# Kernel optimization log

Measured on AMD Instinct MI355X. Metric: run time of the kernel, lower is better.

Reference implementation:

```python
import jax, jax.numpy as jnp
import numpy as np

NUM_CLASSES = 22
H_IMG, W_IMG = 256, 320
VOTE_STEPS = 160          # number of discrete steps each pixel votes along its ray
VOTE_THRESH = 0.5         # inlier threshold used by HoughVoterPyTorch


def setup_inputs() -> dict:
    key = jax.random.key(0)
    ks = jax.random.split(key, 24)
    B = 4
    rn = lambda k, s, sc=1.0: (jax.random.normal(k, s, jnp.float32) * sc)
    inp = {
        'x1': rn(ks[0], (B, 512, 8, 10)),
        'x2': rn(ks[1], (B, 256, 16, 20)),
        'x3': rn(ks[2], (B, 128, 32, 40)),
        'x4': rn(ks[3], (B, 64, 64, 80)),
        'x5': rn(ks[4], (B, 64, 128, 160)),
        'depth': jax.random.uniform(ks[5], (B, 1, H_IMG, W_IMG), jnp.float32, 0.5, 3.0),
    }
    raw = jax.random.uniform(ks[6], (B, NUM_CLASSES, H_IMG, W_IMG), jnp.float32)
    inp['seg'] = jnp.where(raw > 0.97, raw, 0.0)  # sparse per-class responses
    inp['fx'] = jnp.float32(572.4); inp['fy'] = jnp.float32(573.6)
    inp['px'] = jnp.float32(W_IMG / 2); inp['py'] = jnp.float32(H_IMG / 2)
    # ConvTranspose2d weights in torch layout [Cin, Cout, kH, kW]
    inp['w5'] = rn(ks[7], (512, 256, 4, 4), 0.02); inp['b5'] = jnp.zeros((256,), jnp.float32)
    inp['w4'] = rn(ks[8], (512, 128, 4, 4), 0.02); inp['b4'] = jnp.zeros((128,), jnp.float32)
    inp['w3'] = rn(ks[9], (256, 64, 4, 4), 0.03);  inp['b3'] = jnp.zeros((64,), jnp.float32)
    inp['w2'] = rn(ks[10], (128, 64, 4, 4), 0.04); inp['b2'] = jnp.zeros((64,), jnp.float32)
    inp['w1'] = rn(ks[11], (128, 64, 4, 4), 0.04); inp['b1'] = jnp.zeros((64,), jnp.float32)
    inp['wv'] = rn(ks[12], (3 * NUM_CLASSES, 64), 0.1); inp['bv'] = jnp.zeros((3 * NUM_CLASSES,), jnp.float32)
    inp['wc'] = rn(ks[13], (NUM_CLASSES, 64), 0.1);     inp['bc'] = jnp.zeros((NUM_CLASSES,), jnp.float32)
    return inp


def conv_t(x, w, b):
    # torch ConvTranspose2d(k=4, s=2, p=1) == dilated conv with flipped kernel
    k = jnp.flip(w, (2, 3)).transpose(1, 0, 2, 3)  # [Cout, Cin, 4, 4]
    y = jax.lax.conv_general_dilated(x, k, (1, 1), ((2, 2), (2, 2)),
                                     lhs_dilation=(2, 2),
                                     dimension_numbers=('NCHW', 'OIHW', 'NCHW'))
    return y + b[None, :, None, None]


def hough_vote(seg2d, dirs, depth2d, fx, fy, px, py):
    # seg2d: [H,W] fused fg prob; dirs: [H,W,2] (dx,dy); depth2d: [H,W]
    H, W = seg2d.shape
    n = dirs / (jnp.linalg.norm(dirs, axis=-1, keepdims=True) + 1e-6)
    u = n[..., 0].reshape(-1)
    v = n[..., 1].reshape(-1)
    ys, xs = jnp.meshgrid(jnp.arange(H, dtype=jnp.float32),
                          jnp.arange(W, dtype=jnp.float32), indexing='ij')
    xs = xs.reshape(-1); ys = ys.reshape(-1)
    w = (seg2d * (seg2d > VOTE_THRESH)).reshape(-1)  # weighted fg votes

    def step(acc, t):
        xt = jnp.round(xs + t * u).astype(jnp.int32)
        yt = jnp.round(ys + t * v).astype(jnp.int32)
        inb = (xt >= 0) & (xt < W) & (yt >= 0) & (yt < H)
        idx = jnp.clip(yt, 0, H - 1) * W + jnp.clip(xt, 0, W - 1)
        return acc.at[idx].add(jnp.where(inb, w, 0.0)), None

    acc, _ = jax.lax.scan(step, jnp.zeros(H * W, jnp.float32),
                          jnp.arange(1, VOTE_STEPS + 1, dtype=jnp.float32))
    vote_map = acc.reshape(H, W)
    ci = jnp.argmax(acc)
    cy = (ci // W).astype(jnp.float32)
    cx = (ci % W).astype(jnp.float32)
    mask = (seg2d > VOTE_THRESH).astype(jnp.float32)
    tz = jnp.sum(depth2d * mask) / (jnp.sum(mask) + 1e-6)
    tx = (cx - px) * tz / fx
    ty = (cy - py) * tz / fy
    return vote_map, jnp.stack([cx, cy]), jnp.stack([tx, ty, tz])


def reference(x1, x2, x3, x4, x5, depth, seg, fx, fy, px, py,
              w5, b5, w4, b4, w3, b3, w2, b2, w1, b1, wv, bv, wc, bc):
    x = jax.nn.relu(conv_t(x1, w5, b5))
    x = jax.nn.relu(conv_t(jnp.concatenate([x, x2], 1), w4, b4))
    x = jax.nn.relu(conv_t(jnp.concatenate([x, x3], 1), w3, b3))
    x = jax.nn.relu(conv_t(jnp.concatenate([x, x4], 1), w2, b2))
    x = jax.nn.relu(conv_t(jnp.concatenate([x, x5], 1), w1, b1))
    bottom_vertex = jnp.einsum('bchw,oc->bohw', x, wv) + bv[None, :, None, None]
    logits = jnp.einsum('bchw,oc->bohw', x, wc) + bc[None, :, None, None]
    bottom_label = jnp.argmax(logits, axis=1)
    center_dirs = jnp.transpose(bottom_vertex[:, :2], (0, 2, 3, 1))  # [B,H,W,2]
    seg_fused = jnp.clip(jnp.sum(seg, axis=1), 0.0, 1.0)             # [B,H,W]
    vote_maps, centers, translations = jax.vmap(
        hough_vote, in_axes=(0, 0, 0, None, None, None, None)
    )(seg_fused, center_dirs, depth[:, 0], fx, fy, px, py)
    return bottom_vertex, bottom_label, vote_maps, centers, translations
```

## Files before the change

kernel.cpp:

```cpp
#include <hip/hip_runtime.h>
#include <cstdint>
#include <cstddef>

#define H_IMG 256
#define W_IMG 320
#define HW_IMG (H_IMG * W_IMG)
#define NCLS 22
#define VOTE_STEPS 160

__global__ void repack_kernel(const float* __restrict__ w, double* __restrict__ wp,
                              int CIN, int COUT) {
    int total = CIN * COUT * 16;
    for (int i = blockIdx.x * blockDim.x + threadIdx.x; i < total;
         i += gridDim.x * blockDim.x) {
        int j = i & 3;
        int co = (i >> 2) % COUT;
        int rest = (i >> 2) / COUT;
        int cin = rest % CIN;
        int pp = rest / CIN;
        int ry = pp >> 1, rx = pp & 1;
        int dy = j >> 1, dx = j & 1;
        int ky = 3 - ry - 2 * dy;
        int kx = 3 - rx - 2 * dx;
        wp[i] = (double)w[((size_t)cin * COUT + co) * 16 + ky * 4 + kx];
    }
}

__global__ void repackR_kernel(const float* __restrict__ w, double* __restrict__ wr,
                               int CIN, int COUT) {
    int NCOG = COUT >> 4;
    int total = CIN * COUT * 16;
    for (int i = blockIdx.x * blockDim.x + threadIdx.x; i < total;
         i += gridDim.x * blockDim.x) {
        int tap = i & 3;
        int co = (i >> 2) & 15;
        int rest = i >> 6;
        int cin = rest % CIN;
        int pc = rest / CIN;
        int cog = pc % NCOG;
        int pp = pc / NCOG;
        int ry = pp >> 1, rx = pp & 1;
        int dy = tap >> 1, dxx = tap & 1;
        int ky = 3 - ry - 2 * dy;
        int kx = 3 - rx - 2 * dxx;
        wr[i] = (double)w[((size_t)cin * COUT + (cog * 16 + co)) * 16 + ky * 4 + kx];
    }
}

__global__ void transpose_d_kernel(const float* __restrict__ w, double* __restrict__ wt,
                                   int O, int K) {
    int i = blockIdx.x * blockDim.x + threadIdx.x;
    if (i < O * K) {
        int o = i / K, k = i - o * K;
        wt[k * O + o] = (double)w[i];
    }
}

template <bool RELU_A, bool ADBL>
__global__ __launch_bounds__(256) void convt_part_kernel(
    const void* __restrict__ inA_, int CA,
    const float* __restrict__ inB, int CB,
    const double* __restrict__ wp,
    double* __restrict__ parts,
    int COUT, int Hin, int Win, int nSplit, int B, int TOT) {
    const int NCO = 16;
    const int CIN = CA + CB;
    const int cog = blockIdx.y >> 2;
    const int pp = blockIdx.y & 3;
    const int ry = pp >> 1, rx = pp & 1;
    const int b = blockIdx.z % B;
    const int sp = blockIdx.z / B;
    const int cinPer = CIN / nSplit;
    const int c0 = sp * cinPer, c1 = c0 + cinPer;
    const int co0 = cog * NCO;
    const int plane = Hin * Win;
    const int Hout = Hin * 2, Wout = Win * 2;
    double* out = parts + (size_t)sp * TOT;

    __shared__ double wl[64 * 64];
    for (int i = threadIdx.x; i < cinPer * 64; i += 256) {
        int ci = i >> 6, k = i & 63;
        wl[i] = wp[(((size_t)pp * CIN + c0 + ci) * COUT + co0) * 4 + k];
    }
    __syncthreads();

    for (int p = blockIdx.x * 256 + threadIdx.x; p < plane; p += gridDim.x * 256) {
        int m = p / Win, n = p - m * Win;
        int iy0 = m + ry - 1, ix0 = n + rx - 1;
        int oy = 2 * m + ry, ox = 2 * n + rx;
        double f00 = (iy0 >= 0 && ix0 >= 0) ? 1.0 : 0.0;
        double f01 = (iy0 >= 0 && ix0 + 1 < Win) ? 1.0 : 0.0;
        double f10 = (iy0 + 1 < Hin && ix0 >= 0) ? 1.0 : 0.0;
        double f11 = (iy0 + 1 < Hin && ix0 + 1 < Win) ? 1.0 : 0.0;
        int cy0 = max(iy0, 0), cy1 = min(iy0 + 1, Hin - 1);
        int cx0 = max(ix0, 0), cx1 = min(ix0 + 1, Win - 1);
        int o00 = cy0 * Win + cx0, o01 = cy0 * Win + cx1;
        int o10 = cy1 * Win + cx0, o11 = cy1 * Win + cx1;

        double acc[16];
#pragma unroll
        for (int k = 0; k < 16; ++k) acc[k] = 0.0;

        int a0 = min(c0, CA), a1 = min(c1, CA);
        for (int c = a0; c < a1; ++c) {
            double x00, x01, x10, x11;
            if (ADBL) {
                const double* s = (const double*)inA_ + ((size_t)b * CA + c) * plane;
                x00 = f00 * s[o00]; x01 = f01 * s[o01];
                x10 = f10 * s[o10]; x11 = f11 * s[o11];
            } else {
                const float* s = (const float*)inA_ + ((size_t)b * CA + c) * plane;
                x00 = f00 * (double)s[o00]; x01 = f01 * (double)s[o01];
                x10 = f10 * (double)s[o10]; x11 = f11 * (double)s[o11];
            }
            if (RELU_A) {
                x00 = fmax(x00, 0.0); x01 = fmax(x01, 0.0);
                x10 = fmax(x10, 0.0); x11 = fmax(x11, 0.0);
            }
            const double2* w2 = (const double2*)&wl[(c - c0) * 64];
#pragma unroll
            for (int k = 0; k < 16; ++k) {
                double2 wa = w2[k * 2], wb = w2[k * 2 + 1];
                acc[k] += x00 * wa.x + x01 * wa.y + x10 * wb.x + x11 * wb.y;
            }
        }
        if (CB > 0 && c1 > CA) {
            int b0 = max(c0, CA) - CA, b1 = c1 - CA;
            const float* srcB = inB + (size_t)b * CB * plane;
            for (int c = b0; c < b1; ++c) {
                const float* s = srcB + (size_t)c * plane;
                double x00 = f00 * (double)s[o00], x01 = f01 * (double)s[o01];
                double x10 = f10 * (double)s[o10], x11 = f11 * (double)s[o11];
                const double2* w2 = (const double2*)&wl[(c + CA - c0) * 64];
#pragma unroll
                for (int k = 0; k < 16; ++k) {
                    double2 wa = w2[k * 2], wb = w2[k * 2 + 1];
                    acc[k] += x00 * wa.x + x01 * wa.y + x10 * wb.x + x11 * wb.y;
                }
            }
        }

        size_t ob = ((size_t)b * COUT + co0) * (size_t)Hout * Wout +
                    (size_t)oy * Wout + ox;
#pragma unroll
        for (int k = 0; k < 16; ++k)
            out[ob + (size_t)k * Hout * Wout] = acc[k];
    }
}

__global__ void reduce_part_kernel(const double* __restrict__ parts,
                                   const float* __restrict__ bias,
                                   double* __restrict__ out,
                                   int nSplit, int COUT, int HWo, int TOT) {
    int i = blockIdx.x * blockDim.x + threadIdx.x;
    if (i < TOT) {
        double a = (double)bias[(i / HWo) % COUT];
        for (int sp = 0; sp < nSplit; ++sp) a += parts[(size_t)sp * TOT + i];
        out[i] = a;
    }
}

template <int PX>
__global__ __launch_bounds__(256) void convt_reg_kernel(
    const double* __restrict__ zin, const float* __restrict__ xin,
    const double* __restrict__ wr,
    const float* __restrict__ bias,
    double* __restrict__ out,
    int COUT, int Hin, int Win) {
    const int NCOG = COUT >> 4;
    const int plane = Hin * Win;
    const int Wq = Win / PX;
    const int cog = blockIdx.y >> 2, pp = blockIdx.y & 3;
    const int ry = pp >> 1, rx = pp & 1;
    const int b = blockIdx.z;
    __shared__ double wl[4096];

    int t = blockIdx.x * 256 + threadIdx.x;
    int m = t / Wq, n0 = (t - m * Wq) * PX;
    int r0 = m + ry - 1, r1 = r0 + 1;
    double mr0 = (r0 >= 0) ? 1.0 : 0.0;
    double mr1 = (r1 < Hin) ? 1.0 : 0.0;
    int cr0 = max(r0, 0) * Win, cr1 = min(r1, Hin - 1) * Win;
    const int ib = rx ? 0 : 1;
    const int eidx = rx ? PX : 0;
    int eoff = rx ? min(n0 + PX, Win - 1) : max(n0 - 1, 0);
    double me = rx ? ((n0 + PX < Win) ? 1.0 : 0.0) : ((n0 > 0) ? 1.0 : 0.0);
    double me0 = me * mr0, me1 = me * mr1;

    double acc[16][PX];
#pragma unroll
    for (int k = 0; k < 16; ++k) {
        double bvv = (double)bias[cog * 16 + k];
#pragma unroll
        for (int tt = 0; tt < PX; ++tt) acc[k][tt] = bvv;
    }

    const double* wbase = wr + (size_t)(pp * NCOG + cog) * 128 * 64;

    for (int i = threadIdx.x; i < 4096; i += 256) wl[i] = wbase[i];
    __syncthreads();
    {
        const double* s = zin + (size_t)b * 64 * plane;
        for (int c = 0; c < 64; ++c) {
            double xa0[PX + 1], xa1[PX + 1];
#pragma unroll
            for (int j = 0; j < PX / 2; ++j) {
                double2 v0 = *(const double2*)(s + cr0 + n0 + 2 * j);
                double2 v1 = *(const double2*)(s + cr1 + n0 + 2 * j);
                xa0[ib + 2 * j] = mr0 * fmax(v0.x, 0.0);
                xa0[ib + 2 * j + 1] = mr0 * fmax(v0.y, 0.0);
                xa1[ib + 2 * j] = mr1 * fmax(v1.x, 0.0);
                xa1[ib + 2 * j + 1] = mr1 * fmax(v1.y, 0.0);
            }
            xa0[eidx] = me0 * fmax(s[cr0 + eoff], 0.0);
            xa1[eidx] = me1 * fmax(s[cr1 + eoff], 0.0);
            const double2* w2 = (const double2*)&wl[c * 64];
#pragma unroll
            for (int co = 0; co < 16; ++co) {
                double2 wa = w2[co * 2], wb = w2[co * 2 + 1];
#pragma unroll
                for (int tt = 0; tt < PX; ++tt)
                    acc[co][tt] += wa.x * xa0[tt] + wa.y * xa0[tt + 1] +
                                   wb.x * xa1[tt] + wb.y * xa1[tt + 1];
            }
            s += plane;
        }
    }
    __syncthreads();
    for (int i = threadIdx.x; i < 4096; i += 256) wl[i] = wbase[4096 + i];
    __syncthreads();
    {
        const float* s = xin + (size_t)b * 64 * plane;
        for (int c = 0; c < 64; ++c) {
            double xa0[PX + 1], xa1[PX + 1];
#pragma unroll
            for (int j = 0; j < PX / 2; ++j) {
                float2 v0 = *(const float2*)(s + cr0 + n0 + 2 * j);
                float2 v1 = *(const float2*)(s + cr1 + n0 + 2 * j);
                xa0[ib + 2 * j] = mr0 * (double)v0.x;
                xa0[ib + 2 * j + 1] = mr0 * (double)v0.y;
                xa1[ib + 2 * j] = mr1 * (double)v1.x;
                xa1[ib + 2 * j + 1] = mr1 * (double)v1.y;
            }
            xa0[eidx] = me0 * (double)s[cr0 + eoff];
            xa1[eidx] = me1 * (double)s[cr1 + eoff];
            const double2* w2 = (const double2*)&wl[c * 64];
#pragma unroll
            for (int co = 0; co < 16; ++co) {
                double2 wa = w2[co * 2], wb = w2[co * 2 + 1];
#pragma unroll
                for (int tt = 0; tt < PX; ++tt)
                    acc[co][tt] += wa.x * xa0[tt] + wa.y * xa0[tt + 1] +
                                   wb.x * xa1[tt] + wb.y * xa1[tt + 1];
            }
            s += plane;
        }
    }

    int oy = 2 * m + ry;
    size_t ob = (size_t)(b * COUT + cog * 16) * plane * 4 + (size_t)oy * (Win * 2);
#pragma unroll
    for (int co = 0; co < 16; ++co)
#pragma unroll
        for (int tt = 0; tt < PX; ++tt)
            out[ob + (size_t)co * plane * 4 + 2 * (n0 + tt) + rx] = acc[co][tt];
}

__global__ __launch_bounds__(256) void head_lds_kernel(
    const double* __restrict__ z5,
    const double* __restrict__ wvT,
    const float* __restrict__ bv,
    const double* __restrict__ wcT,
    const float* __restrict__ bc,
    float* __restrict__ vert, double* __restrict__ dirs,
    float* __restrict__ label) {
    int p = blockIdx.x * 256 + threadIdx.x;
    int half = blockIdx.y;
    int b = blockIdx.z;
    __shared__ double wl[64 * 44];
    if (half == 0) {
        for (int i = threadIdx.x; i < 64 * 44; i += 256) {
            int c = i / 44, k = i - c * 44;
            wl[i] = wvT[c * 66 + k];
        }
    } else {
        for (int i = threadIdx.x; i < 64 * 44; i += 256) {
            int c = i / 44, k = i - c * 44;
            wl[i] = (k < 22) ? wvT[c * 66 + 44 + k] : wcT[c * 22 + (k - 22)];
        }
    }
    __syncthreads();

    const double* xp = z5 + (size_t)b * 64 * HW_IMG + p;
    if (half == 0) {
        double acc[44];
#pragma unroll
        for (int k = 0; k < 44; ++k) acc[k] = (double)bv[k];
        for (int c = 0; c < 64; ++c) {
            double x = fmax(xp[(size_t)c * HW_IMG], 0.0);
            const double2* w2 = (const double2*)&wl[c * 44];
#pragma unroll
            for (int j = 0; j < 22; ++j) {
                double2 w = w2[j];
                acc[2 * j] += x * w.x; acc[2 * j + 1] += x * w.y;
            }
        }
        float* op = vert + (size_t)b * 66 * HW_IMG + p;
#pragma unroll
        for (int k = 0; k < 44; ++k) op[(size_t)k * HW_IMG] = (float)acc[k];
        dirs[(size_t)b * 2 * HW_IMG + p] = acc[0];
        dirs[(size_t)b * 2 * HW_IMG + HW_IMG + p] = acc[1];
    } else {
        double acc[22], lg[22];
#pragma unroll
        for (int k = 0; k < 22; ++k) { acc[k] = (double)bv[44 + k]; lg[k] = (double)bc[k]; }
        for (int c = 0; c < 64; ++c) {
            double x = fmax(xp[(size_t)c * HW_IMG], 0.0);
            const double2* w2 = (const double2*)&wl[c * 44];
#pragma unroll
            for (int j = 0; j < 11; ++j) {
                double2 w = w2[j];
                acc[2 * j] += x * w.x; acc[2 * j + 1] += x * w.y;
            }
#pragma unroll
            for (int j = 0; j < 11; ++j) {
                double2 w = w2[11 + j];
                lg[2 * j] += x * w.x; lg[2 * j + 1] += x * w.y;
            }
        }
        float* op = vert + ((size_t)b * 66 + 44) * HW_IMG + p;
#pragma unroll
        for (int k = 0; k < 22; ++k) op[(size_t)k * HW_IMG] = (float)acc[k];
        int bi = 0; double bvv = lg[0];
#pragma unroll
        for (int k = 1; k < 22; ++k)
            if (lg[k] > bvv) { bvv = lg[k]; bi = k; }
        label[(size_t)b * HW_IMG + p] = (float)bi;
    }
}

__global__ __launch_bounds__(256) void vote_d_kernel(
    const float* __restrict__ seg, const float* __restrict__ depth,
    const double* __restrict__ dirs, double* __restrict__ voteacc,
    double* __restrict__ sums) {
    int p = blockIdx.x * 256 + threadIdx.x;
    int b = blockIdx.z;
    double s = 0.0;
    const float* sp = seg + (size_t)b * NCLS * HW_IMG + p;
    for (int c = 0; c < NCLS; ++c) s += (double)sp[(size_t)c * HW_IMG];
    s = fmin(fmax(s, 0.0), 1.0);
    bool msk = s > 0.5;
    double d = (double)depth[(size_t)b * HW_IMG + p];
    double dm = msk ? d : 0.0;
    double mm = msk ? 1.0 : 0.0;
    for (int off = 32; off > 0; off >>= 1) {
        dm += __shfl_down(dm, off);
        mm += __shfl_down(mm, off);
    }
    __shared__ double sdm[4], smm[4];
    int wid = threadIdx.x >> 6, lane = threadIdx.x & 63;
    if (lane == 0) { sdm[wid] = dm; smm[wid] = mm; }
    __syncthreads();
    if (threadIdx.x == 0) {
        atomicAdd(&sums[b * 2 + 0], sdm[0] + sdm[1] + sdm[2] + sdm[3]);
        atomicAdd(&sums[b * 2 + 1], smm[0] + smm[1] + smm[2] + smm[3]);
    }
    if (msk) {
        double dx = dirs[(size_t)b * 2 * HW_IMG + p];
        double dy = dirs[(size_t)b * 2 * HW_IMG + HW_IMG + p];
        double nrm = sqrt(dx * dx + dy * dy) + 1e-6;
        double u = dx / nrm, v = dy / nrm;
        double xf = (double)(p % W_IMG), yf = (double)(p / W_IMG);
        double tmax = 1e30;
        if (u > 1e-9)       tmax = fmin(tmax, ((double)W_IMG - 0.25 - xf) / u);
        else if (u < -1e-9) tmax = fmin(tmax, (-0.75 - xf) / u);
        if (v > 1e-9)       tmax = fmin(tmax, ((double)H_IMG - 0.25 - yf) / v);
        else if (v < -1e-9) tmax = fmin(tmax, (-0.75 - yf) / v);
        int nst = VOTE_STEPS;
        if (tmax < (double)VOTE_STEPS) nst = (int)tmax + 1;
        double* vb = voteacc + (size_t)b * HW_IMG;
        for (int t = 1; t <= nst; ++t) {
            double tf = (double)t;
            int xi = (int)rint(xf + tf * u);
            int yi = (int)rint(yf + tf * v);
            if (xi >= 0 && xi < W_IMG && yi >= 0 && yi < H_IMG)
                atomicAdd(&vb[yi * W_IMG + xi], s);
        }
    }
}

__global__ void vote_cvt_kernel(const double* __restrict__ voteacc,
                                float* __restrict__ vote, int total) {
    int i = blockIdx.x * blockDim.x + threadIdx.x;
    if (i < total) vote[i] = (float)voteacc[i];
}

__global__ __launch_bounds__(1024) void center_d_kernel(
    const double* __restrict__ voteacc, const double* __restrict__ sums,
    const float* __restrict__ fx, const float* __restrict__ fy,
    const float* __restrict__ px, const float* __restrict__ py,
    float* __restrict__ centers, float* __restrict__ transl) {
    int b = blockIdx.x;
    const double* vb = voteacc + (size_t)b * HW_IMG;
    double best = -1.0;
    int bi = HW_IMG;
    for (int i = threadIdx.x; i < HW_IMG; i += 1024) {
        double v = vb[i];
        if (v > best || (v == best && i < bi)) { best = v; bi = i; }
    }
    for (int off = 32; off > 0; off >>= 1) {
        double ov = __shfl_down(best, off);
        int oi = __shfl_down(bi, off);
        if (ov > best || (ov == best && oi < bi)) { best = ov; bi = oi; }
    }
    __shared__ double sbv[16];
    __shared__ int sbi[16];
    int wid = threadIdx.x >> 6, lane = threadIdx.x & 63;
    if (lane == 0) { sbv[wid] = best; sbi[wid] = bi; }
    __syncthreads();
    if (threadIdx.x == 0) {
        for (int q = 1; q < 16; ++q)
            if (sbv[q] > best || (sbv[q] == best && sbi[q] < bi)) {
                best = sbv[q]; bi = sbi[q];
            }
        double cx = (double)(bi % W_IMG), cy = (double)(bi / W_IMG);
        double tz = sums[b * 2 + 0] / (sums[b * 2 + 1] + 1e-6);
        double tx = (cx - (double)px[0]) * tz / (double)fx[0];
        double ty = (cy - (double)py[0]) * tz / (double)fy[0];
        centers[b * 2 + 0] = (float)cx;
        centers[b * 2 + 1] = (float)cy;
        transl[b * 3 + 0] = (float)tx;
        transl[b * 3 + 1] = (float)ty;
        transl[b * 3 + 2] = (float)tz;
    }
}

extern "C" void kernel_launch(void* const* d_in, const int* in_sizes, int n_in,
                              void* d_out, int out_size, void* d_ws, size_t ws_size,
                              hipStream_t stream) {
    const float* x1 = (const float*)d_in[0];
    const float* x2 = (const float*)d_in[1];
    const float* x3 = (const float*)d_in[2];
    const float* x4 = (const float*)d_in[3];
    const float* x5 = (const float*)d_in[4];
    const float* depth = (const float*)d_in[5];
    const float* seg = (const float*)d_in[6];
    const float* fx = (const float*)d_in[7];
    const float* fy = (const float*)d_in[8];
    const float* px = (const float*)d_in[9];
    const float* py = (const float*)d_in[10];
    const float* w5 = (const float*)d_in[11];
    const float* b5 = (const float*)d_in[12];
    const float* w4 = (const float*)d_in[13];
    const float* b4 = (const float*)d_in[14];
    const float* w3 = (const float*)d_in[15];
    const float* b3 = (const float*)d_in[16];
    const float* w2 = (const float*)d_in[17];
    const float* b2 = (const float*)d_in[18];
    const float* w1 = (const float*)d_in[19];
    const float* b1 = (const float*)d_in[20];
    const float* wv = (const float*)d_in[21];
    const float* bv = (const float*)d_in[22];
    const float* wc = (const float*)d_in[23];
    const float* bc = (const float*)d_in[24];

    float* out = (float*)d_out;
    float* vert = out;
    float* label = vert + (size_t)4 * 66 * HW_IMG;
    float* vote = label + (size_t)4 * HW_IMG;
    float* centers = vote + (size_t)4 * HW_IMG;
    float* transl = centers + 8;

    double* zA = (double*)d_ws;
    double* zB = zA + 20971520;
    double* dirs = zB + 5242880;
    double* voteacc = dirs + 655360;
    double* sums = voteacc + 327680;
    double* wp5 = sums + 8;
    double* wp4 = wp5 + 2097152;
    double* wp3 = wp4 + 1048576;
    double* wr2 = wp3 + 262144;
    double* wr1 = wr2 + 131072;
    double* wvT = wr1 + 131072;
    double* wcT = wvT + 4224;
    double* z1 = zA; double* z2 = zB; double* z3 = zA; double* z4 = zB; double* z5 = zA;
    double* parts = zA + 2000000;

    hipMemsetAsync(voteacc, 0, (327680 + 8) * sizeof(double), stream);

    auto rp = [&](const float* w, double* wp, int CIN, int COUT) {
        int total = CIN * COUT * 16;
        repack_kernel<<<(total + 255) / 256, 256, 0, stream>>>(w, wp, CIN, COUT);
    };
    rp(w5, wp5, 512, 256);
    rp(w4, wp4, 512, 128);
    rp(w3, wp3, 256, 64);
    repackR_kernel<<<(131072 + 255) / 256, 256, 0, stream>>>(w2, wr2, 128, 64);
    repackR_kernel<<<(131072 + 255) / 256, 256, 0, stream>>>(w1, wr1, 128, 64);
    transpose_d_kernel<<<(66 * 64 + 255) / 256, 256, 0, stream>>>(wv, wvT, 66, 64);
    transpose_d_kernel<<<(22 * 64 + 255) / 256, 256, 0, stream>>>(wc, wcT, 22, 64);

    convt_part_kernel<false, false><<<dim3(1, 64, 32), 256, 0, stream>>>(
        x1, 512, nullptr, 0, wp5, parts, 256, 8, 10, 8, 4, 327680);
    reduce_part_kernel<<<1280, 256, 0, stream>>>(parts, b5, z1, 8, 256, 320, 327680);
    convt_part_kernel<true, true><<<dim3(2, 32, 32), 256, 0, stream>>>(
        z1, 256, x2, 256, wp4, parts, 128, 16, 20, 8, 4, 655360);
    reduce_part_kernel<<<2560, 256, 0, stream>>>(parts, b4, z2, 8, 128, 1280, 655360);
    convt_part_kernel<true, true><<<dim3(5, 16, 16), 256, 0, stream>>>(
        z2, 128, x3, 128, wp3, parts, 64, 32, 40, 4, 4, 1310720);
    reduce_part_kernel<<<5120, 256, 0, stream>>>(parts, b3, z3, 4, 64, 5120, 1310720);
    convt_reg_kernel<2><<<dim3(10, 16, 4), 256, 0, stream>>>(
        z3, x4, wr2, b2, z4, 64, 64, 80);
    convt_reg_kernel<2><<<dim3(40, 16, 4), 256, 0, stream>>>(
        z4, x5, wr1, b1, z5, 64, 128, 160);

    head_lds_kernel<<<dim3(320, 2, 4), 256, 0, stream>>>(z5, wvT, bv, wcT, bc,
                                                         vert, dirs, label);

    vote_d_kernel<<<dim3(320, 1, 4), 256, 0, stream>>>(seg, depth, dirs, voteacc, sums);
    vote_cvt_kernel<<<(327680 + 255) / 256, 256, 0, stream>>>(voteacc, vote, 327680);
    center_d_kernel<<<4, 1024, 0, stream>>>(voteacc, sums, fx, fy, px, py, centers, transl);
}
```

Before: 2.431 ms.

## Tile Hough voting into LDS accumulators with per-chunk partials and reduction

Splits voting into a prep kernel that stores per-pixel ray parameters, a tiled kernel that clips each ray to a 64x64 tile and accumulates votes with shared-memory atomics, and a reduce kernel that sums the chunk partials and writes both the double and float vote maps. This replaces contended global double atomics with LDS atomics. In exchange every (chunk, tile) block rescans its chunk's rays, which adds ray reloads and clipping work, plus a partial buffer of 16 chunks × 4 batches × 20 tiles to reduce.

After: 1.955 ms. -19.6%, faster.

```diff
diff --git a/kernel.cpp b/kernel.cpp
--- a/kernel.cpp
+++ b/kernel.cpp
@@ -7,6 +7,13 @@
 #define HW_IMG (H_IMG * W_IMG)
 #define NCLS 22
 #define VOTE_STEPS 160
+#define TW 64
+#define TH 64
+#define NTX 5
+#define NTY 4
+#define NTILE (NTX * NTY)
+#define NCHUNK 16
+#define CHPIX (HW_IMG / NCHUNK)
 
 __global__ void repack_kernel(const float* __restrict__ w, double* __restrict__ wp,
                               int CIN, int COUT) {
@@ -339,9 +346,12 @@
     }
 }
 
-__global__ __launch_bounds__(256) void vote_d_kernel(
+__global__ __launch_bounds__(256) void vote_prep_kernel(
     const float* __restrict__ seg, const float* __restrict__ depth,
-    const double* __restrict__ dirs, double* __restrict__ voteacc,
+    const double* __restrict__ dirs,
+    double* __restrict__ rayS, double* __restrict__ rayU,
+    double* __restrict__ rayV, double* __restrict__ rayRU,
+    double* __restrict__ rayRV, double* __restrict__ rayN,
     double* __restrict__ sums) {
     int p = blockIdx.x * 256 + threadIdx.x;
     int b = blockIdx.z;
@@ -365,6 +375,7 @@
         atomicAdd(&sums[b * 2 + 0], sdm[0] + sdm[1] + sdm[2] + sdm[3]);
         atomicAdd(&sums[b * 2 + 1], smm[0] + smm[1] + smm[2] + smm[3]);
     }
+    size_t idx = (size_t)b * HW_IMG + p;
     if (msk) {
         double dx = dirs[(size_t)b * 2 * HW_IMG + p];
         double dy = dirs[(size_t)b * 2 * HW_IMG + HW_IMG + p];
@@ -378,21 +389,87 @@
         else if (v < -1e-9) tmax = fmin(tmax, (-0.75 - yf) / v);
         int nst = VOTE_STEPS;
         if (tmax < (double)VOTE_STEPS) nst = (int)tmax + 1;
-        double* vb = voteacc + (size_t)b * HW_IMG;
-        for (int t = 1; t <= nst; ++t) {
+        rayS[idx] = s;
+        rayU[idx] = u;
+        rayV[idx] = v;
+        rayRU[idx] = (u != 0.0) ? 1.0 / u : 0.0;
+        rayRV[idx] = (v != 0.0) ? 1.0 / v : 0.0;
+        rayN[idx] = (double)nst;
+    } else {
+        rayS[idx] = 0.0;
+    }
+}
+
+__global__ __launch_bounds__(256) void vote_tile_kernel(
+    const double* __restrict__ rayS, const double* __restrict__ rayU,
+    const double* __restrict__ rayV, const double* __restrict__ rayRU,
+    const double* __restrict__ rayRV, const double* __restrict__ rayN,
+    double* __restrict__ vparts) {
+    int chunk = blockIdx.x;
+    int tile = blockIdx.y;
+    int b = blockIdx.z;
+    int tx0 = (tile % NTX) * TW, ty0 = (tile / NTX) * TH;
+    __shared__ double vt[TW * TH];
+    for (int i = threadIdx.x; i < TW * TH; i += 256) vt[i] = 0.0;
+    __syncthreads();
+
+    size_t base = (size_t)b * HW_IMG;
+    int p0 = chunk * CHPIX;
+    for (int q = threadIdx.x; q < CHPIX; q += 256) {
+        int p = p0 + q;
+        double s = rayS[base + p];
+        if (s == 0.0) continue;
+        double u = rayU[base + p], v = rayV[base + p];
+        double ru = rayRU[base + p], rv = rayRV[base + p];
+        int nst = (int)rayN[base + p];
+        double xf = (double)(p % W_IMG), yf = (double)(p / W_IMG);
+        double ta = 1.0, tb = (double)nst;
+        if (ru != 0.0) {
+            double lo = ((double)(tx0 - 1) - xf) * ru;
+            double hi = ((double)(tx0 + TW) - xf) * ru;
+            ta = fmax(ta, fmin(lo, hi));
+            tb = fmin(tb, fmax(lo, hi));
+        } else {
+            if (xf < (double)(tx0 - 1) || xf > (double)(tx0 + TW)) continue;
+        }
+        if (rv != 0.0) {
+            double lo = ((double)(ty0 - 1) - yf) * rv;
+            double hi = ((double)(ty0 + TH) - yf) * rv;
+            ta = fmax(ta, fmin(lo, hi));
+            tb = fmin(tb, fmax(lo, hi));
+        } else {
+            if (yf < (double)(ty0 - 1) || yf > (double)(ty0 + TH)) continue;
+        }
+        if (ta > tb) continue;
+        int t0 = (int)ceil(ta), t1 = (int)floor(tb);
+        for (int t = t0; t <= t1; ++t) {
             double tf = (double)t;
             int xi = (int)rint(xf + tf * u);
             int yi = (int)rint(yf + tf * v);
-            if (xi >= 0 && xi < W_IMG && yi >= 0 && yi < H_IMG)
-                atomicAdd(&vb[yi * W_IMG + xi], s);
-        }
-    }
-}
-
-__global__ void vote_cvt_kernel(const double* __restrict__ voteacc,
-                                float* __restrict__ vote, int total) {
-    int i = blockIdx.x * blockDim.x + threadIdx.x;
-    if (i < total) vote[i] = (float)voteacc[i];
+            if (xi >= tx0 && xi < tx0 + TW && yi >= ty0 && yi < ty0 + TH)
+                atomicAdd(&vt[(yi - ty0) * TW + (xi - tx0)], s);
+        }
+    }
+    __syncthreads();
+    double* dst = vparts + (((size_t)chunk * 4 + b) * NTILE + tile) * (TW * TH);
+    for (int i = threadIdx.x; i < TW * TH; i += 256) dst[i] = vt[i];
+}
+
+__global__ void vote_reduce_kernel(const double* __restrict__ vparts,
+                                   double* __restrict__ voteacc,
+                                   float* __restrict__ vote) {
+    int i = blockIdx.x * 256 + threadIdx.x;
+    if (i < 4 * HW_IMG) {
+        int b = i / HW_IMG, cell = i - b * HW_IMG;
+        int y = cell / W_IMG, x = cell - y * W_IMG;
+        int tile = (y / TH) * NTX + (x / TW);
+        int ci = (y % TH) * TW + (x % TW);
+        double a = 0.0;
+        for (int c = 0; c < NCHUNK; ++c)
+            a += vparts[(((size_t)c * 4 + b) * NTILE + tile) * (TW * TH) + ci];
+        voteacc[i] = a;
+        vote[i] = (float)a;
+    }
 }
 
 __global__ __launch_bounds__(1024) void center_d_kernel(
@@ -485,8 +562,15 @@
     double* wcT = wvT + 4224;
     double* z1 = zA; double* z2 = zB; double* z3 = zA; double* z4 = zB; double* z5 = zA;
     double* parts = zA + 2000000;
-
-    hipMemsetAsync(voteacc, 0, (327680 + 8) * sizeof(double), stream);
+    double* rayS = zB;
+    double* rayU = zB + 327680;
+    double* rayV = zB + 2 * 327680;
+    double* rayRU = zB + 3 * 327680;
+    double* rayRV = zB + 4 * 327680;
+    double* rayN = zB + 5 * 327680;
+    double* vparts = zA;
+
+    hipMemsetAsync(sums, 0, 8 * sizeof(double), stream);
 
     auto rp = [&](const float* w, double* wp, int CIN, int COUT) {
         int total = CIN * COUT * 16;
@@ -517,7 +601,12 @@
     head_lds_kernel<<<dim3(320, 2, 4), 256, 0, stream>>>(z5, wvT, bv, wcT, bc,
                                                          vert, dirs, label);
 
-    vote_d_kernel<<<dim3(320, 1, 4), 256, 0, stream>>>(seg, depth, dirs, voteacc, sums);
-    vote_cvt_kernel<<<(327680 + 255) / 256, 256, 0, stream>>>(voteacc, vote, 327680);
-    center_d_kernel<<<4, 1024, 0, stream>>>(voteacc, sums, fx, fy, px, py, centers, transl);
-}
+    vote_prep_kernel<<<dim3(320, 1, 4), 256, 0, stream>>>(
+        seg, depth, dirs, rayS, rayU, rayV, rayRU, rayRV, rayN, sums);
+    vote_tile_kernel<<<dim3(NCHUNK, NTILE, 4), 256, 0, stream>>>(
+        rayS, rayU, rayV, rayRU, rayRV, rayN, vparts);
+    vote_reduce_kernel<<<(4 * HW_IMG + 255) / 256, 256, 0, stream>>>(
+        vparts, voteacc, vote);
+    center_d_kernel<<<4, 1024, 0, stream>>>(voteacc, sums, fx, fy, px, py,
+                                            centers, transl);
+}
```
